# Optimization experiments

Hardware: AMD Instinct MI355X
Metric: run time of the kernel (lower is better)

## Reference

```python
import jax, jax.numpy as jnp
import numpy as np

B, S, D, H = 8, 2048, 1024, 4
HD = D // H


def _layernorm(x, w, b, eps=1e-5):
    mu = jnp.mean(x, axis=-1, keepdims=True)
    var = jnp.mean((x - mu) ** 2, axis=-1, keepdims=True)
    return (x - mu) * jax.lax.rsqrt(var + eps) * w + b


def setup_inputs() -> dict:
    key = jax.random.key(0)
    ks = jax.random.split(key, 10)
    s = 1.0 / np.sqrt(D)
    return {
        "text_representation": jax.random.normal(ks[0], (B, S, D), jnp.float32),
        "image_representation": jax.random.normal(ks[1], (B, S, D), jnp.float32),
        "ln_t_w": jnp.ones((D,), jnp.float32),
        "ln_t_b": jnp.zeros((D,), jnp.float32),
        "ln_i_w": jnp.ones((D,), jnp.float32),
        "ln_i_b": jnp.zeros((D,), jnp.float32),
        "Wa": jax.random.uniform(ks[2], (H, HD, D), jnp.float32, -s, s),
        "Wa_b": jax.random.uniform(ks[3], (H, HD), jnp.float32, -s, s),
        "Wq": jax.random.uniform(ks[4], (H, HD, D), jnp.float32, -s, s),
        "Wq_b": jax.random.uniform(ks[5], (H, HD), jnp.float32, -s, s),
        "sim_w": jax.random.uniform(ks[6], (HD, 1), jnp.float32, -1.0, 1.0),
        "sim_b": jax.random.uniform(ks[7], (HD,), jnp.float32, -1.0, 1.0),
        "fc_w": jax.random.uniform(ks[8], (1, H * HD), jnp.float32, -s, s),
        "fc_b": jax.random.uniform(ks[9], (1,), jnp.float32, -s, s),
    }


def reference(text_representation, image_representation, ln_t_w, ln_t_b,
              ln_i_w, ln_i_b, Wa, Wa_b, Wq, Wq_b, sim_w, sim_b, fc_w, fc_b):
    eps_cos = 1e-6
    text_rep = _layernorm(text_representation, ln_t_w, ln_t_b)   # [B,S,D]
    image_rep = _layernorm(image_representation, ln_i_w, ln_i_b)  # [B,S,D]
    # cosine similarity along last dim (torch-style norm clamping)
    tn = jnp.maximum(jnp.linalg.norm(text_rep, axis=-1), eps_cos)
    im = jnp.maximum(jnp.linalg.norm(image_rep, axis=-1), eps_cos)
    per_pos_sim = jnp.sum(text_rep * image_rep, axis=-1) / (tn * im)  # [B,S]
    global_sim = jnp.mean(per_pos_sim, axis=1, keepdims=True)          # [B,1]
    text_global = jnp.mean(text_rep, axis=1)    # [B,D]
    image_global = jnp.mean(image_rep, axis=1)  # [B,D]
    gate_a = jnp.einsum('bd,hkd->bhk', text_global, Wa) + Wa_b    # [B,H,HD]
    gate_q = jnp.einsum('bd,hkd->bhk', image_global, Wq) + Wq_b   # [B,H,HD]
    sim_feat = global_sim * sim_w[:, 0] + sim_b                   # [B,HD]
    gates = jax.nn.relu(gate_a + gate_q + sim_feat[:, None, :])   # [B,H,HD]
    combined = gates.reshape(gates.shape[0], H * HD)              # [B,H*HD]
    final_gate = jax.nn.sigmoid(combined @ fc_w.T + fc_b)         # [B,1]
    g = final_gate[:, :, None]                                    # [B,1,1]
    return g * text_rep + (1.0 - g) * image_rep
```

## Files before the change

kernel.cpp:

```cpp
#include <hip/hip_runtime.h>
#include <hip/hip_cooperative_groups.h>
#include <math.h>

namespace cg = cooperative_groups;

#define BB 8
#define SS 2048
#define DD 1024
#define HH 4
#define HDD 256
#define NROW (BB*SS)

#define GG 32
#define NBLK (NROW/GG)
#define NSL  (NBLK*4)

#define OFF_PT 0
#define OFF_PI (OFF_PT + NSL*DD)
#define OFF_PS (OFF_PI + NSL*DD)
#define OFF_TG (OFF_PS + NSL)
#define OFF_IG (OFF_TG + BB*DD)
#define OFF_SIM (OFF_IG + BB*DD)
#define OFF_LOGIT (OFF_SIM + BB)

#define GF 8
#define NSLF (NROW/GF)
#define F_MU_T 0
#define F_RS_T NROW
#define F_MU_I (2*NROW)
#define F_RS_I (3*NROW)
#define F_PT   (4*NROW)
#define F_PI   (F_PT + NSLF*DD)
#define F_PS   (F_PI + NSLF*DD)
#define F_TG   (F_PS + NSLF)
#define F_IG   (F_TG + BB*DD)
#define F_SIM  (F_IG + BB*DD)
#define F_LOGIT (F_SIM + BB)

__device__ __forceinline__ float wred(float v) {
#pragma unroll
  for (int m = 32; m > 0; m >>= 1) v += __shfl_xor(v, m, 64);
  return v;
}
__device__ __forceinline__ float hsum(const float4 v) { return v.x+v.y+v.z+v.w; }
__device__ __forceinline__ float hsq(const float4 v)  { return v.x*v.x+v.y*v.y+v.z*v.z+v.w*v.w; }
__device__ __forceinline__ float hdot(const float4 a, const float4 b) {
  return a.x*b.x + a.y*b.y + a.z*b.z + a.w*b.w;
}

__global__ __launch_bounds__(256, 2) void fused(
    const float* __restrict__ text, const float* __restrict__ image,
    const float* __restrict__ wt, const float* __restrict__ bt,
    const float* __restrict__ wi, const float* __restrict__ bi,
    const float* __restrict__ Wa, const float* __restrict__ Wab,
    const float* __restrict__ Wq, const float* __restrict__ Wqb,
    const float* __restrict__ simw, const float* __restrict__ simb,
    const float* __restrict__ fcw, const float* __restrict__ fcb,
    float* __restrict__ ws, float* __restrict__ out)
{
  cg::grid_group grid = cg::this_grid();
  const int blk  = blockIdx.x;
  const int tid  = threadIdx.x;
  const int lane = tid & 63;
  const int wv   = tid >> 6;
  const int row0 = blk * GG;

  __shared__ float smu_t[GG], srs_t[GG], smu_i[GG], srs_i[GG];
  __shared__ float sred[2][8][32];
  __shared__ float red3[4][4][BB];

  {
    const int cb = lane << 2;
    float4 Wt[4], Bt[4], Wi4[4], Bi4[4];
#pragma unroll
    for (int j = 0; j < 4; ++j) {
      Wt[j]  = *(const float4*)(wt + j*256 + cb);
      Bt[j]  = *(const float4*)(bt + j*256 + cb);
      Wi4[j] = *(const float4*)(wi + j*256 + cb);
      Bi4[j] = *(const float4*)(bi + j*256 + cb);
    }
    float4 tga[4], iga[4];
#pragma unroll
    for (int j = 0; j < 4; ++j) {
      tga[j] = make_float4(0.f,0.f,0.f,0.f);
      iga[j] = make_float4(0.f,0.f,0.f,0.f);
    }
    float sim_loc = 0.f;
    const float invD = 1.f/DD;
    const int rbase = row0 + wv*8;

#pragma unroll 1
    for (int r = 0; r < 8; ++r) {
      const float* trow = text  + (size_t)(rbase + r)*DD + cb;
      const float* irow = image + (size_t)(rbase + r)*DD + cb;
      float4 t[4], im[4];
#pragma unroll
      for (int j = 0; j < 4; ++j) t[j]  = *(const float4*)(trow + j*256);
#pragma unroll
      for (int j = 0; j < 4; ++j) im[j] = *(const float4*)(irow + j*256);

      float st=0.f, qt=0.f, si=0.f, qi=0.f;
#pragma unroll
      for (int j = 0; j < 4; ++j) {
        st += hsum(t[j]);  qt += hsq(t[j]);
        si += hsum(im[j]); qi += hsq(im[j]);
      }
      st = wred(st); qt = wred(qt); si = wred(si); qi = wred(qi);
      const float mt = st*invD, rt = rsqrtf(qt*invD - mt*mt + 1e-5f);
      const float mi = si*invD, ri = rsqrtf(qi*invD - mi*mi + 1e-5f);
      if (lane == 0) {
        smu_t[wv*8+r]=mt; srs_t[wv*8+r]=rt;
        smu_i[wv*8+r]=mi; srs_i[wv*8+r]=ri;
      }

      float dot=0.f, nt=0.f, ni=0.f;
#pragma unroll
      for (int j = 0; j < 4; ++j) {
        float4 tn, iv;
        tn.x = (t[j].x-mt)*rt*Wt[j].x + Bt[j].x;
        tn.y = (t[j].y-mt)*rt*Wt[j].y + Bt[j].y;
        tn.z = (t[j].z-mt)*rt*Wt[j].z + Bt[j].z;
        tn.w = (t[j].w-mt)*rt*Wt[j].w + Bt[j].w;
        iv.x = (im[j].x-mi)*ri*Wi4[j].x + Bi4[j].x;
        iv.y = (im[j].y-mi)*ri*Wi4[j].y + Bi4[j].y;
        iv.z = (im[j].z-mi)*ri*Wi4[j].z + Bi4[j].z;
        iv.w = (im[j].w-mi)*ri*Wi4[j].w + Bi4[j].w;
        tga[j].x += tn.x; tga[j].y += tn.y; tga[j].z += tn.z; tga[j].w += tn.w;
        iga[j].x += iv.x; iga[j].y += iv.y; iga[j].z += iv.z; iga[j].w += iv.w;
        dot += hdot(tn, iv); nt += hsq(tn); ni += hsq(iv);
      }
      dot = wred(dot); nt = wred(nt); ni = wred(ni);
      sim_loc += dot / (fmaxf(sqrtf(nt),1e-6f) * fmaxf(sqrtf(ni),1e-6f));
    }

    const int slice = blk*4 + wv;
#pragma unroll
    for (int j = 0; j < 4; ++j) {
      *(float4*)(ws + OFF_PT + (size_t)slice*DD + j*256 + cb) = tga[j];
      *(float4*)(ws + OFF_PI + (size_t)slice*DD + j*256 + cb) = iga[j];
    }
    if (lane == 0) ws[OFF_PS + slice] = sim_loc;
  }

  grid.sync();

  if (blk < 256) {
    const int b   = blk >> 5;
    const int ch  = blk & 31;
    const int cl  = tid & 31;
    const int sg  = tid >> 5;
    const int col = ch*32 + cl;
    const float* pt = ws + OFF_PT + (size_t)(b*256 + sg*32)*DD + col;
    const float* pi = ws + OFF_PI + (size_t)(b*256 + sg*32)*DD + col;
    float at = 0.f, ai = 0.f;
#pragma unroll 4
    for (int k = 0; k < 32; ++k) {
      at += pt[(size_t)k*DD];
      ai += pi[(size_t)k*DD];
    }
    sred[0][sg][cl] = at;
    sred[1][sg][cl] = ai;
    __syncthreads();
    if (tid < 32) {
      float v = 0.f;
#pragma unroll
      for (int q = 0; q < 8; ++q) v += sred[0][q][tid];
      ws[OFF_TG + b*DD + ch*32 + tid] = v;
    } else if (tid < 64) {
      const int c = tid - 32;
      float v = 0.f;
#pragma unroll
      for (int q = 0; q < 8; ++q) v += sred[1][q][c];
      ws[OFF_IG + b*DD + ch*32 + c] = v;
    }
  } else if (blk == 256) {
    float* sflat = (float*)sred;
    const int b = tid >> 5, j = tid & 31;
    float a = 0.f;
#pragma unroll
    for (int k = 0; k < 8; ++k) a += ws[OFF_PS + b*256 + j*8 + k];
    sflat[tid] = a;
    __syncthreads();
    if (j == 0) {
      float ssum = 0.f;
#pragma unroll
      for (int m = 0; m < 32; ++m) ssum += sflat[b*32 + m];
      ws[OFF_SIM + b] = ssum;
    }
    if (tid < BB) ws[OFF_LOGIT + tid] = 0.f;
  }

  grid.sync();

  if (blk < 256) {
    const int d0 = tid << 2;
    const int r0 = blk * 4;
    for (int rr = 0; rr < 4; ++rr) {
      const int r = r0 + rr;
      const float4 a4 = *(const float4*)(Wa + (size_t)r*DD + d0);
      const float4 q4 = *(const float4*)(Wq + (size_t)r*DD + d0);
      float acc[BB];
#pragma unroll
      for (int b = 0; b < BB; ++b) {
        const float4 t = *(const float4*)(ws + OFF_TG + b*DD + d0);
        const float4 i = *(const float4*)(ws + OFF_IG + b*DD + d0);
        acc[b] = hdot(a4, t) + hdot(q4, i);
      }
#pragma unroll
      for (int b = 0; b < BB; ++b) {
        acc[b] = wred(acc[b]);
        if (lane == 0) red3[rr][wv][b] = acc[b];
      }
    }
    __syncthreads();
    if (tid < BB) {
      const int b = tid;
      const float inv = 1.f/SS;
      const float gs = ws[OFF_SIM + b] * inv;
      float part = 0.f;
#pragma unroll
      for (int rr = 0; rr < 4; ++rr) {
        const int r = r0 + rr;
        const int k = r & 255;
        const float v = (red3[rr][0][b] + red3[rr][1][b] + red3[rr][2][b] + red3[rr][3][b]) * inv;
        float gate = v + Wab[r] + Wqb[r] + gs*simw[k] + simb[k];
        gate = fmaxf(gate, 0.f);
        part += gate * fcw[r];
      }
      atomicAdd(&ws[OFF_LOGIT + b], part);
    }
  }

  grid.sync();

  {
    const int d0 = tid << 2;
    const float4 wt4 = *(const float4*)(wt + d0);
    const float4 bt4 = *(const float4*)(bt + d0);
    const float4 wi4 = *(const float4*)(wi + d0);
    const float4 bi4 = *(const float4*)(bi + d0);
    const int b = row0 >> 11;
    const float g  = 1.f / (1.f + expf(-(ws[OFF_LOGIT + b] + fcb[0])));
    const float gi = 1.f - g;
#pragma unroll 1
    for (int rr = 0; rr < GG; rr += 4) {
      float4 t[4], im[4];
#pragma unroll
      for (int r = 0; r < 4; ++r) {
        t[r]  = *(const float4*)(text  + (size_t)(row0+rr+r)*DD + d0);
        im[r] = *(const float4*)(image + (size_t)(row0+rr+r)*DD + d0);
      }
#pragma unroll
      for (int r = 0; r < 4; ++r) {
        const float mt = smu_t[rr+r], rt = srs_t[rr+r];
        const float mi = smu_i[rr+r], ri = srs_i[rr+r];
        const float gt = g*rt, gii = gi*ri;
        float4 o;
        o.x = gt*(t[r].x-mt)*wt4.x + g*bt4.x + gii*(im[r].x-mi)*wi4.x + gi*bi4.x;
        o.y = gt*(t[r].y-mt)*wt4.y + g*bt4.y + gii*(im[r].y-mi)*wi4.y + gi*bi4.y;
        o.z = gt*(t[r].z-mt)*wt4.z + g*bt4.z + gii*(im[r].z-mi)*wi4.z + gi*bi4.z;
        o.w = gt*(t[r].w-mt)*wt4.w + g*bt4.w + gii*(im[r].w-mi)*wi4.w + gi*bi4.w;
        *(float4*)(out + (size_t)(row0+rr+r)*DD + d0) = o;
      }
    }
  }
}

__global__ __launch_bounds__(256) void k1_stats(
    const float* __restrict__ text, const float* __restrict__ image,
    const float* __restrict__ wt, const float* __restrict__ bt,
    const float* __restrict__ wi, const float* __restrict__ bi,
    float* __restrict__ ws)
{
  const int g    = blockIdx.x;
  const int tid  = threadIdx.x;
  const int lane = tid & 63;
  const int wv   = tid >> 6;
  const int d0   = tid << 2;
  const int row0 = g * GF;

  __shared__ float red1[4][8];
  __shared__ float red2[4][6];

  const float4 wt4 = *(const float4*)(wt + d0);
  const float4 bt4 = *(const float4*)(bt + d0);
  const float4 wi4 = *(const float4*)(wi + d0);
  const float4 bi4 = *(const float4*)(bi + d0);

  float4 tga = make_float4(0.f,0.f,0.f,0.f);
  float4 iga = make_float4(0.f,0.f,0.f,0.f);
  float sim_loc = 0.f;

  for (int r = 0; r < GF; r += 2) {
    const size_t base0 = (size_t)(row0 + r) * DD + d0;
    const size_t base1 = base0 + DD;
    const float4 t0 = *(const float4*)(text  + base0);
    const float4 i0 = *(const float4*)(image + base0);
    const float4 t1 = *(const float4*)(text  + base1);
    const float4 i1 = *(const float4*)(image + base1);

    float a0 = hsum(t0), a1 = hsq(t0), a2 = hsum(i0), a3 = hsq(i0);
    float a4 = hsum(t1), a5 = hsq(t1), a6 = hsum(i1), a7 = hsq(i1);
    a0 = wred(a0); a1 = wred(a1); a2 = wred(a2); a3 = wred(a3);
    a4 = wred(a4); a5 = wred(a5); a6 = wred(a6); a7 = wred(a7);
    if (lane == 0) {
      red1[wv][0]=a0; red1[wv][1]=a1; red1[wv][2]=a2; red1[wv][3]=a3;
      red1[wv][4]=a4; red1[wv][5]=a5; red1[wv][6]=a6; red1[wv][7]=a7;
    }
    __syncthreads();
    float s[8];
#pragma unroll
    for (int q = 0; q < 8; ++q) s[q] = red1[0][q]+red1[1][q]+red1[2][q]+red1[3][q];
    const float invD = 1.f/DD;
    const float mt0 = s[0]*invD, rt0 = rsqrtf(s[1]*invD - mt0*mt0 + 1e-5f);
    const float mi0 = s[2]*invD, ri0 = rsqrtf(s[3]*invD - mi0*mi0 + 1e-5f);
    const float mt1 = s[4]*invD, rt1 = rsqrtf(s[5]*invD - mt1*mt1 + 1e-5f);
    const float mi1 = s[6]*invD, ri1 = rsqrtf(s[7]*invD - mi1*mi1 + 1e-5f);
    if (tid == 0) {
      const int row = row0 + r;
      ws[F_MU_T+row]=mt0;   ws[F_RS_T+row]=rt0;
      ws[F_MU_I+row]=mi0;   ws[F_RS_I+row]=ri0;
      ws[F_MU_T+row+1]=mt1; ws[F_RS_T+row+1]=rt1;
      ws[F_MU_I+row+1]=mi1; ws[F_RS_I+row+1]=ri1;
    }
    float4 tn0, in0, tn1, in1;
    tn0.x = (t0.x-mt0)*rt0*wt4.x + bt4.x;  tn0.y = (t0.y-mt0)*rt0*wt4.y + bt4.y;
    tn0.z = (t0.z-mt0)*rt0*wt4.z + bt4.z;  tn0.w = (t0.w-mt0)*rt0*wt4.w + bt4.w;
    in0.x = (i0.x-mi0)*ri0*wi4.x + bi4.x;  in0.y = (i0.y-mi0)*ri0*wi4.y + bi4.y;
    in0.z = (i0.z-mi0)*ri0*wi4.z + bi4.z;  in0.w = (i0.w-mi0)*ri0*wi4.w + bi4.w;
    tn1.x = (t1.x-mt1)*rt1*wt4.x + bt4.x;  tn1.y = (t1.y-mt1)*rt1*wt4.y + bt4.y;
    tn1.z = (t1.z-mt1)*rt1*wt4.z + bt4.z;  tn1.w = (t1.w-mt1)*rt1*wt4.w + bt4.w;
    in1.x = (i1.x-mi1)*ri1*wi4.x + bi4.x;  in1.y = (i1.y-mi1)*ri1*wi4.y + bi4.y;
    in1.z = (i1.z-mi1)*ri1*wi4.z + bi4.z;  in1.w = (i1.w-mi1)*ri1*wi4.w + bi4.w;

    tga.x += tn0.x + tn1.x; tga.y += tn0.y + tn1.y;
    tga.z += tn0.z + tn1.z; tga.w += tn0.w + tn1.w;
    iga.x += in0.x + in1.x; iga.y += in0.y + in1.y;
    iga.z += in0.z + in1.z; iga.w += in0.w + in1.w;

    float b0 = hdot(tn0,in0), b1 = hsq(tn0), b2 = hsq(in0);
    float b3 = hdot(tn1,in1), b4 = hsq(tn1), b5 = hsq(in1);
    b0 = wred(b0); b1 = wred(b1); b2 = wred(b2);
    b3 = wred(b3); b4 = wred(b4); b5 = wred(b5);
    if (lane == 0) {
      red2[wv][0]=b0; red2[wv][1]=b1; red2[wv][2]=b2;
      red2[wv][3]=b3; red2[wv][4]=b4; red2[wv][5]=b5;
    }
    __syncthreads();
    if (tid == 0) {
      float u[6];
#pragma unroll
      for (int q = 0; q < 6; ++q) u[q] = red2[0][q]+red2[1][q]+red2[2][q]+red2[3][q];
      sim_loc += u[0] / (fmaxf(sqrtf(u[1]),1e-6f) * fmaxf(sqrtf(u[2]),1e-6f));
      sim_loc += u[3] / (fmaxf(sqrtf(u[4]),1e-6f) * fmaxf(sqrtf(u[5]),1e-6f));
    }
  }
  *(float4*)(ws + F_PT + (size_t)g*DD + d0) = tga;
  *(float4*)(ws + F_PI + (size_t)g*DD + d0) = iga;
  if (tid == 0) ws[F_PS + g] = sim_loc;
}

__global__ __launch_bounds__(256) void kR_reduce(float* __restrict__ ws)
{
  const int tid = threadIdx.x;
  if (blockIdx.x < 256) {
    const int b   = blockIdx.x >> 5;
    const int ch  = blockIdx.x & 31;
    const int cl  = tid & 31;
    const int sg  = tid >> 5;
    const int col = ch*32 + cl;
    const float* pt = ws + F_PT + (size_t)(b*256 + sg*32)*DD + col;
    const float* pi = ws + F_PI + (size_t)(b*256 + sg*32)*DD + col;
    float at = 0.f, ai = 0.f;
#pragma unroll 4
    for (int k = 0; k < 32; ++k) {
      at += pt[(size_t)k*DD];
      ai += pi[(size_t)k*DD];
    }
    __shared__ float sred[2][8][32];
    sred[0][sg][cl] = at;
    sred[1][sg][cl] = ai;
    __syncthreads();
    if (tid < 32) {
      float v = 0.f;
#pragma unroll
      for (int q = 0; q < 8; ++q) v += sred[0][q][tid];
      ws[F_TG + b*DD + ch*32 + tid] = v;
    } else if (tid < 64) {
      const int c = tid - 32;
      float v = 0.f;
#pragma unroll
      for (int q = 0; q < 8; ++q) v += sred[1][q][c];
      ws[F_IG + b*DD + ch*32 + c] = v;
    }
  } else {
    __shared__ float sred[256];
    const int b = tid >> 5, j = tid & 31;
    float a = 0.f;
#pragma unroll
    for (int k = 0; k < 8; ++k) a += ws[F_PS + b*256 + j*8 + k];
    sred[tid] = a;
    __syncthreads();
    if (j == 0) {
      float s = 0.f;
#pragma unroll
      for (int m = 0; m < 32; ++m) s += sred[b*32 + m];
      ws[F_SIM + b] = s;
    }
    if (tid < BB) ws[F_LOGIT + tid] = 0.f;
  }
}

__global__ __launch_bounds__(256) void k2_gates(
    const float* __restrict__ Wa, const float* __restrict__ Wab,
    const float* __restrict__ Wq, const float* __restrict__ Wqb,
    const float* __restrict__ simw, const float* __restrict__ simb,
    const float* __restrict__ fcw, float* __restrict__ ws)
{
  const int tid  = threadIdx.x;
  const int lane = tid & 63;
  const int wv   = tid >> 6;
  const int r0   = blockIdx.x * 4;
  const int d0   = tid << 2;

  __shared__ float red[4][4][BB];

  for (int rr = 0; rr < 4; ++rr) {
    const int r = r0 + rr;
    const float4 a4 = *(const float4*)(Wa + (size_t)r*DD + d0);
    const float4 q4 = *(const float4*)(Wq + (size_t)r*DD + d0);
    float acc[BB];
#pragma unroll
    for (int b = 0; b < BB; ++b) {
      const float4 t = *(const float4*)(ws + F_TG + b*DD + d0);
      const float4 i = *(const float4*)(ws + F_IG + b*DD + d0);
      acc[b] = hdot(a4, t) + hdot(q4, i);
    }
#pragma unroll
    for (int b = 0; b < BB; ++b) {
      acc[b] = wred(acc[b]);
      if (lane == 0) red[rr][wv][b] = acc[b];
    }
  }
  __syncthreads();
  if (tid < BB) {
    const int b = tid;
    const float inv = 1.f/SS;
    const float gs = ws[F_SIM + b] * inv;
    float part = 0.f;
#pragma unroll
    for (int rr = 0; rr < 4; ++rr) {
      const int r = r0 + rr;
      const int k = r & 255;
      const float v = (red[rr][0][b] + red[rr][1][b] + red[rr][2][b] + red[rr][3][b]) * inv;
      float gate = v + Wab[r] + Wqb[r] + gs*simw[k] + simb[k];
      gate = fmaxf(gate, 0.f);
      part += gate * fcw[r];
    }
    atomicAdd(&ws[F_LOGIT + b], part);
  }
}

__global__ __launch_bounds__(256) void k3_blend(
    const float* __restrict__ text, const float* __restrict__ image,
    const float* __restrict__ wt, const float* __restrict__ bt,
    const float* __restrict__ wi, const float* __restrict__ bi,
    const float* __restrict__ fcb,
    const float* __restrict__ ws, float* __restrict__ out)
{
  const int r0 = blockIdx.x * 4;
  const int b  = r0 >> 11;
  const int d0 = threadIdx.x << 2;

  float4 t[4], im[4];
#pragma unroll
  for (int r = 0; r < 4; ++r) {
    t[r]  = *(const float4*)(text  + (size_t)(r0+r)*DD + d0);
    im[r] = *(const float4*)(image + (size_t)(r0+r)*DD + d0);
  }
  const float4 wt4 = *(const float4*)(wt + d0);
  const float4 bt4 = *(const float4*)(bt + d0);
  const float4 wi4 = *(const float4*)(wi + d0);
  const float4 bi4 = *(const float4*)(bi + d0);

  const float g  = 1.f / (1.f + expf(-(ws[F_LOGIT+b] + fcb[0])));
  const float gi = 1.f - g;

#pragma unroll
  for (int r = 0; r < 4; ++r) {
    const float mt = ws[F_MU_T+r0+r], rt = ws[F_RS_T+r0+r];
    const float mi = ws[F_MU_I+r0+r], ri = ws[F_RS_I+r0+r];
    const float gt = g*rt, gii = gi*ri;
    float4 o;
    o.x = gt*(t[r].x-mt)*wt4.x + g*bt4.x + gii*(im[r].x-mi)*wi4.x + gi*bi4.x;
    o.y = gt*(t[r].y-mt)*wt4.y + g*bt4.y + gii*(im[r].y-mi)*wi4.y + gi*bi4.y;
    o.z = gt*(t[r].z-mt)*wt4.z + g*bt4.z + gii*(im[r].z-mi)*wi4.z + gi*bi4.z;
    o.w = gt*(t[r].w-mt)*wt4.w + g*bt4.w + gii*(im[r].w-mi)*wi4.w + gi*bi4.w;
    *(float4*)(out + (size_t)(r0+r)*DD + d0) = o;
  }
}

extern "C" void kernel_launch(void* const* d_in, const int* in_sizes, int n_in,
                              void* d_out, int out_size, void* d_ws, size_t ws_size,
                              hipStream_t stream)
{
  const float* text   = (const float*)d_in[0];
  const float* image  = (const float*)d_in[1];
  const float* ln_t_w = (const float*)d_in[2];
  const float* ln_t_b = (const float*)d_in[3];
  const float* ln_i_w = (const float*)d_in[4];
  const float* ln_i_b = (const float*)d_in[5];
  const float* Wa     = (const float*)d_in[6];
  const float* Wab    = (const float*)d_in[7];
  const float* Wq     = (const float*)d_in[8];
  const float* Wqb    = (const float*)d_in[9];
  const float* simw   = (const float*)d_in[10];
  const float* simb   = (const float*)d_in[11];
  const float* fcw    = (const float*)d_in[12];
  const float* fcb    = (const float*)d_in[13];
  float* ws  = (float*)d_ws;
  float* out = (float*)d_out;

  static int use_coop = -1;
  if (use_coop != 0) {
    void* args[16] = {
      (void*)&text, (void*)&image, (void*)&ln_t_w, (void*)&ln_t_b,
      (void*)&ln_i_w, (void*)&ln_i_b, (void*)&Wa, (void*)&Wab,
      (void*)&Wq, (void*)&Wqb, (void*)&simw, (void*)&simb,
      (void*)&fcw, (void*)&fcb, (void*)&ws, (void*)&out
    };
    hipError_t e = hipLaunchCooperativeKernel((void*)fused, dim3(NBLK), dim3(256),
                                              args, 0, stream);
    if (e == hipSuccess) { use_coop = 1; return; }
    use_coop = 0;
  }

  k1_stats<<<NSLF, 256, 0, stream>>>(text, image, ln_t_w, ln_t_b, ln_i_w, ln_i_b, ws);
  kR_reduce<<<257, 256, 0, stream>>>(ws);
  k2_gates<<<HH*HDD/4, 256, 0, stream>>>(Wa, Wab, Wq, Wqb, simw, simb, fcw, ws);
  k3_blend<<<NROW/4, 256, 0, stream>>>(text, image, ln_t_w, ln_t_b, ln_i_w, ln_i_b, fcb, ws, out);
}
```

Baseline: 244.0 us.

## Replace cooperative grid syncs with atomic counters and in-block global reductions

Removes the cooperative-groups grid syncs and the per-slice partial-sum workspace. Each block now reduces its four waves' column sums in shared memory and atomically adds them into per-batch global accumulators. Two global arrival counters with spin-waits replace the grid barriers. Both row loops gain double-buffered register prefetch. A memset clears the accumulators each call, which adds a launch, and the spin-wait relies on the cooperative launch guaranteeing all blocks are co-resident.

```diff
diff --git a/kernel.cpp b/kernel.cpp
--- a/kernel.cpp
+++ b/kernel.cpp
@@ -1,8 +1,5 @@
 #include <hip/hip_runtime.h>
-#include <hip/hip_cooperative_groups.h>
 #include <math.h>
-
-namespace cg = cooperative_groups;
 
 #define BB 8
 #define SS 2048
@@ -13,15 +10,13 @@
 
 #define GG 32
 #define NBLK (NROW/GG)
-#define NSL  (NBLK*4)
-
-#define OFF_PT 0
-#define OFF_PI (OFF_PT + NSL*DD)
-#define OFF_PS (OFF_PI + NSL*DD)
-#define OFF_TG (OFF_PS + NSL)
-#define OFF_IG (OFF_TG + BB*DD)
-#define OFF_SIM (OFF_IG + BB*DD)
+
+#define OFF_TG    0
+#define OFF_IG    (BB*DD)
+#define OFF_SIM   (2*BB*DD)
 #define OFF_LOGIT (OFF_SIM + BB)
+#define OFF_CNT   (OFF_LOGIT + BB)
+#define WS_CLEAR  (OFF_CNT + 2)
 
 #define GF 8
 #define NSLF (NROW/GF)
@@ -58,16 +53,20 @@
     const float* __restrict__ fcw, const float* __restrict__ fcb,
     float* __restrict__ ws, float* __restrict__ out)
 {
-  cg::grid_group grid = cg::this_grid();
   const int blk  = blockIdx.x;
   const int tid  = threadIdx.x;
   const int lane = tid & 63;
   const int wv   = tid >> 6;
   const int row0 = blk * GG;
+  const int b    = blk >> 6;
 
   __shared__ float smu_t[GG], srs_t[GG], smu_i[GG], srs_i[GG];
-  __shared__ float sred[2][8][32];
+  __shared__ float sAcc[2][4][DD];
+  __shared__ float ssim[4];
   __shared__ float red3[4][4][BB];
+
+  int* c1 = (int*)(ws + OFF_CNT);
+  int* c2 = c1 + 1;
 
   {
     const int cb = lane << 2;
@@ -89,21 +88,35 @@
     const float invD = 1.f/DD;
     const int rbase = row0 + wv*8;
 
-#pragma unroll 1
+    float4 tb[2][4], ib[2][4];
+    {
+      const float* tr = text  + (size_t)rbase*DD + cb;
+      const float* ir = image + (size_t)rbase*DD + cb;
+#pragma unroll
+      for (int j = 0; j < 4; ++j) {
+        tb[0][j] = *(const float4*)(tr + j*256);
+        ib[0][j] = *(const float4*)(ir + j*256);
+      }
+    }
+
+#pragma unroll 2
     for (int r = 0; r < 8; ++r) {
-      const float* trow = text  + (size_t)(rbase + r)*DD + cb;
-      const float* irow = image + (size_t)(rbase + r)*DD + cb;
-      float4 t[4], im[4];
-#pragma unroll
-      for (int j = 0; j < 4; ++j) t[j]  = *(const float4*)(trow + j*256);
-#pragma unroll
-      for (int j = 0; j < 4; ++j) im[j] = *(const float4*)(irow + j*256);
+      const int cur = r & 1, nxt = cur ^ 1;
+      if (r < 7) {
+        const float* tr = text  + (size_t)(rbase + r + 1)*DD + cb;
+        const float* ir = image + (size_t)(rbase + r + 1)*DD + cb;
+#pragma unroll
+        for (int j = 0; j < 4; ++j) {
+          tb[nxt][j] = *(const float4*)(tr + j*256);
+          ib[nxt][j] = *(const float4*)(ir + j*256);
+        }
+      }
 
       float st=0.f, qt=0.f, si=0.f, qi=0.f;
 #pragma unroll
       for (int j = 0; j < 4; ++j) {
-        st += hsum(t[j]);  qt += hsq(t[j]);
-        si += hsum(im[j]); qi += hsq(im[j]);
+        st += hsum(tb[cur][j]);  qt += hsq(tb[cur][j]);
+        si += hsum(ib[cur][j]);  qi += hsq(ib[cur][j]);
       }
       st = wred(st); qt = wred(qt); si = wred(si); qi = wred(qi);
       const float mt = st*invD, rt = rsqrtf(qt*invD - mt*mt + 1e-5f);
@@ -117,14 +130,14 @@
 #pragma unroll
       for (int j = 0; j < 4; ++j) {
         float4 tn, iv;
-        tn.x = (t[j].x-mt)*rt*Wt[j].x + Bt[j].x;
-        tn.y = (t[j].y-mt)*rt*Wt[j].y + Bt[j].y;
-        tn.z = (t[j].z-mt)*rt*Wt[j].z + Bt[j].z;
-        tn.w = (t[j].w-mt)*rt*Wt[j].w + Bt[j].w;
-        iv.x = (im[j].x-mi)*ri*Wi4[j].x + Bi4[j].x;
-        iv.y = (im[j].y-mi)*ri*Wi4[j].y + Bi4[j].y;
-        iv.z = (im[j].z-mi)*ri*Wi4[j].z + Bi4[j].z;
-        iv.w = (im[j].w-mi)*ri*Wi4[j].w + Bi4[j].w;
+        tn.x = (tb[cur][j].x-mt)*rt*Wt[j].x + Bt[j].x;
+        tn.y = (tb[cur][j].y-mt)*rt*Wt[j].y + Bt[j].y;
+        tn.z = (tb[cur][j].z-mt)*rt*Wt[j].z + Bt[j].z;
+        tn.w = (tb[cur][j].w-mt)*rt*Wt[j].w + Bt[j].w;
+        iv.x = (ib[cur][j].x-mi)*ri*Wi4[j].x + Bi4[j].x;
+        iv.y = (ib[cur][j].y-mi)*ri*Wi4[j].y + Bi4[j].y;
+        iv.z = (ib[cur][j].z-mi)*ri*Wi4[j].z + Bi4[j].z;
+        iv.w = (ib[cur][j].w-mi)*ri*Wi4[j].w + Bi4[j].w;
         tga[j].x += tn.x; tga[j].y += tn.y; tga[j].z += tn.z; tga[j].w += tn.w;
         iga[j].x += iv.x; iga[j].y += iv.y; iga[j].z += iv.z; iga[j].w += iv.w;
         dot += hdot(tn, iv); nt += hsq(tn); ni += hsq(iv);
@@ -133,66 +146,50 @@
       sim_loc += dot / (fmaxf(sqrtf(nt),1e-6f) * fmaxf(sqrtf(ni),1e-6f));
     }
 
-    const int slice = blk*4 + wv;
 #pragma unroll
     for (int j = 0; j < 4; ++j) {
-      *(float4*)(ws + OFF_PT + (size_t)slice*DD + j*256 + cb) = tga[j];
-      *(float4*)(ws + OFF_PI + (size_t)slice*DD + j*256 + cb) = iga[j];
-    }
-    if (lane == 0) ws[OFF_PS + slice] = sim_loc;
-  }
-
-  grid.sync();
+      *(float4*)&sAcc[0][wv][j*256 + cb] = tga[j];
+      *(float4*)&sAcc[1][wv][j*256 + cb] = iga[j];
+    }
+    if (lane == 0) ssim[wv] = sim_loc;
+    __syncthreads();
+
+    const int c0 = tid << 2;
+    float4 vt = make_float4(0.f,0.f,0.f,0.f);
+    float4 vi = make_float4(0.f,0.f,0.f,0.f);
+#pragma unroll
+    for (int w = 0; w < 4; ++w) {
+      const float4 a = *(const float4*)&sAcc[0][w][c0];
+      vt.x += a.x; vt.y += a.y; vt.z += a.z; vt.w += a.w;
+      const float4 e = *(const float4*)&sAcc[1][w][c0];
+      vi.x += e.x; vi.y += e.y; vi.z += e.z; vi.w += e.w;
+    }
+    atomicAdd(&ws[OFF_TG + b*DD + c0 + 0], vt.x);
+    atomicAdd(&ws[OFF_TG + b*DD + c0 + 1], vt.y);
+    atomicAdd(&ws[OFF_TG + b*DD + c0 + 2], vt.z);
+    atomicAdd(&ws[OFF_TG + b*DD + c0 + 3], vt.w);
+    atomicAdd(&ws[OFF_IG + b*DD + c0 + 0], vi.x);
+    atomicAdd(&ws[OFF_IG + b*DD + c0 + 1], vi.y);
+    atomicAdd(&ws[OFF_IG + b*DD + c0 + 2], vi.z);
+    atomicAdd(&ws[OFF_IG + b*DD + c0 + 3], vi.w);
+    if (tid == 0) {
+      atomicAdd(&ws[OFF_SIM + b], ssim[0]+ssim[1]+ssim[2]+ssim[3]);
+    }
+  }
+
+  __syncthreads();
+  if (tid == 0) {
+    __hip_atomic_fetch_add(c1, 1, __ATOMIC_RELEASE, __HIP_MEMORY_SCOPE_AGENT);
+  }
 
   if (blk < 256) {
-    const int b   = blk >> 5;
-    const int ch  = blk & 31;
-    const int cl  = tid & 31;
-    const int sg  = tid >> 5;
-    const int col = ch*32 + cl;
-    const float* pt = ws + OFF_PT + (size_t)(b*256 + sg*32)*DD + col;
-    const float* pi = ws + OFF_PI + (size_t)(b*256 + sg*32)*DD + col;
-    float at = 0.f, ai = 0.f;
-#pragma unroll 4
-    for (int k = 0; k < 32; ++k) {
-      at += pt[(size_t)k*DD];
-      ai += pi[(size_t)k*DD];
-    }
-    sred[0][sg][cl] = at;
-    sred[1][sg][cl] = ai;
-    __syncthreads();
-    if (tid < 32) {
-      float v = 0.f;
-#pragma unroll
-      for (int q = 0; q < 8; ++q) v += sred[0][q][tid];
-      ws[OFF_TG + b*DD + ch*32 + tid] = v;
-    } else if (tid < 64) {
-      const int c = tid - 32;
-      float v = 0.f;
-#pragma unroll
-      for (int q = 0; q < 8; ++q) v += sred[1][q][c];
-      ws[OFF_IG + b*DD + ch*32 + c] = v;
-    }
-  } else if (blk == 256) {
-    float* sflat = (float*)sred;
-    const int b = tid >> 5, j = tid & 31;
-    float a = 0.f;
-#pragma unroll
-    for (int k = 0; k < 8; ++k) a += ws[OFF_PS + b*256 + j*8 + k];
-    sflat[tid] = a;
-    __syncthreads();
-    if (j == 0) {
-      float ssum = 0.f;
-#pragma unroll
-      for (int m = 0; m < 32; ++m) ssum += sflat[b*32 + m];
-      ws[OFF_SIM + b] = ssum;
-    }
-    if (tid < BB) ws[OFF_LOGIT + tid] = 0.f;
-  }
-
-  grid.sync();
-
-  if (blk < 256) {
+    if (tid == 0) {
+      while (__hip_atomic_load(c1, __ATOMIC_RELAXED, __HIP_MEMORY_SCOPE_AGENT) < NBLK)
+        __builtin_amdgcn_s_sleep(8);
+      __threadfence();
+    }
+    __syncthreads();
+
     const int d0 = tid << 2;
     const int r0 = blk * 4;
     for (int rr = 0; rr < 4; ++rr) {
@@ -201,37 +198,46 @@
       const float4 q4 = *(const float4*)(Wq + (size_t)r*DD + d0);
       float acc[BB];
 #pragma unroll
-      for (int b = 0; b < BB; ++b) {
-        const float4 t = *(const float4*)(ws + OFF_TG + b*DD + d0);
-        const float4 i = *(const float4*)(ws + OFF_IG + b*DD + d0);
-        acc[b] = hdot(a4, t) + hdot(q4, i);
-      }
-#pragma unroll
-      for (int b = 0; b < BB; ++b) {
-        acc[b] = wred(acc[b]);
-        if (lane == 0) red3[rr][wv][b] = acc[b];
+      for (int bq = 0; bq < BB; ++bq) {
+        const float4 t = *(const float4*)(ws + OFF_TG + bq*DD + d0);
+        const float4 i = *(const float4*)(ws + OFF_IG + bq*DD + d0);
+        acc[bq] = hdot(a4, t) + hdot(q4, i);
+      }
+#pragma unroll
+      for (int bq = 0; bq < BB; ++bq) {
+        acc[bq] = wred(acc[bq]);
+        if (lane == 0) red3[rr][wv][bq] = acc[bq];
       }
     }
     __syncthreads();
     if (tid < BB) {
-      const int b = tid;
+      const int bq = tid;
       const float inv = 1.f/SS;
-      const float gs = ws[OFF_SIM + b] * inv;
+      const float gs = ws[OFF_SIM + bq] * inv;
       float part = 0.f;
 #pragma unroll
       for (int rr = 0; rr < 4; ++rr) {
         const int r = r0 + rr;
         const int k = r & 255;
-        const float v = (red3[rr][0][b] + red3[rr][1][b] + red3[rr][2][b] + red3[rr][3][b]) * inv;
+        const float v = (red3[rr][0][bq] + red3[rr][1][bq] + red3[rr][2][bq] + red3[rr][3][bq]) * inv;
         float gate = v + Wab[r] + Wqb[r] + gs*simw[k] + simb[k];
         gate = fmaxf(gate, 0.f);
         part += gate * fcw[r];
       }
-      atomicAdd(&ws[OFF_LOGIT + b], part);
-    }
-  }
-
-  grid.sync();
+      atomicAdd(&ws[OFF_LOGIT + bq], part);
+    }
+    __syncthreads();
+    if (tid == 0) {
+      __hip_atomic_fetch_add(c2, 1, __ATOMIC_RELEASE, __HIP_MEMORY_SCOPE_AGENT);
+    }
+  }
+
+  if (tid == 0) {
+    while (__hip_atomic_load(c2, __ATOMIC_RELAXED, __HIP_MEMORY_SCOPE_AGENT) < 256)
+      __builtin_amdgcn_s_sleep(8);
+    __threadfence();
+  }
+  __syncthreads();
 
   {
     const int d0 = tid << 2;
@@ -239,27 +245,37 @@
     const float4 bt4 = *(const float4*)(bt + d0);
     const float4 wi4 = *(const float4*)(wi + d0);
     const float4 bi4 = *(const float4*)(bi + d0);
-    const int b = row0 >> 11;
     const float g  = 1.f / (1.f + expf(-(ws[OFF_LOGIT + b] + fcb[0])));
     const float gi = 1.f - g;
-#pragma unroll 1
-    for (int rr = 0; rr < GG; rr += 4) {
-      float4 t[4], im[4];
-#pragma unroll
-      for (int r = 0; r < 4; ++r) {
-        t[r]  = *(const float4*)(text  + (size_t)(row0+rr+r)*DD + d0);
-        im[r] = *(const float4*)(image + (size_t)(row0+rr+r)*DD + d0);
-      }
+
+    float4 tg[2][4], ig[2][4];
+#pragma unroll
+    for (int r = 0; r < 4; ++r) {
+      tg[0][r] = *(const float4*)(text  + (size_t)(row0+r)*DD + d0);
+      ig[0][r] = *(const float4*)(image + (size_t)(row0+r)*DD + d0);
+    }
+#pragma unroll 2
+    for (int gidx = 0; gidx < 8; ++gidx) {
+      const int cur = gidx & 1, nxt = cur ^ 1;
+      if (gidx < 7) {
+        const int nr = row0 + (gidx+1)*4;
+#pragma unroll
+        for (int r = 0; r < 4; ++r) {
+          tg[nxt][r] = *(const float4*)(text  + (size_t)(nr+r)*DD + d0);
+          ig[nxt][r] = *(const float4*)(image + (size_t)(nr+r)*DD + d0);
+        }
+      }
+      const int rr = gidx*4;
 #pragma unroll
       for (int r = 0; r < 4; ++r) {
         const float mt = smu_t[rr+r], rt = srs_t[rr+r];
         const float mi = smu_i[rr+r], ri = srs_i[rr+r];
         const float gt = g*rt, gii = gi*ri;
         float4 o;
-        o.x = gt*(t[r].x-mt)*wt4.x + g*bt4.x + gii*(im[r].x-mi)*wi4.x + gi*bi4.x;
-        o.y = gt*(t[r].y-mt)*wt4.y + g*bt4.y + gii*(im[r].y-mi)*wi4.y + gi*bi4.y;
-        o.z = gt*(t[r].z-mt)*wt4.z + g*bt4.z + gii*(im[r].z-mi)*wi4.z + gi*bi4.z;
-        o.w = gt*(t[r].w-mt)*wt4.w + g*bt4.w + gii*(im[r].w-mi)*wi4.w + gi*bi4.w;
+        o.x = gt*(tg[cur][r].x-mt)*wt4.x + g*bt4.x + gii*(ig[cur][r].x-mi)*wi4.x + gi*bi4.x;
+        o.y = gt*(tg[cur][r].y-mt)*wt4.y + g*bt4.y + gii*(ig[cur][r].y-mi)*wi4.y + gi*bi4.y;
+        o.z = gt*(tg[cur][r].z-mt)*wt4.z + g*bt4.z + gii*(ig[cur][r].z-mi)*wi4.z + gi*bi4.z;
+        o.w = gt*(tg[cur][r].w-mt)*wt4.w + g*bt4.w + gii*(ig[cur][r].w-mi)*wi4.w + gi*bi4.w;
         *(float4*)(out + (size_t)(row0+rr+r)*DD + d0) = o;
       }
     }
@@ -521,6 +537,8 @@
   float* ws  = (float*)d_ws;
   float* out = (float*)d_out;
 
+  hipMemsetAsync(ws, 0, WS_CLEAR * sizeof(float), stream);
+
   static int use_coop = -1;
   if (use_coop != 0) {
     void* args[16] = {
```

Result: no change. 248.4 us (+1.8%).
